# Performance work log

Measured on AMD Instinct MI355X. Metric: run time of the kernel, lower is better.

The kernel has to match this reference:

```python
import jax, jax.numpy as jnp
import numpy as np

NUM_CLASSES = 1000
DENSE_DIM = 64 * 64  # 4096, hardcoded in the module
BATCH = 8192
W0, W1 = 0.5, 0.5  # self.weights


def setup_inputs() -> dict:
    key = jax.random.key(0)
    k1, k2, k3, k4 = jax.random.split(key, 4)
    logits = jax.random.normal(k1, (BATCH, NUM_CLASSES), dtype=jnp.float32)
    dense_out = jax.random.normal(k2, (BATCH, DENSE_DIM), dtype=jnp.float32)
    target = jax.random.randint(k3, (BATCH,), 0, NUM_CLASSES, dtype=jnp.int32)
    # dense_labels buffer: random 0/1 per (class, dense) cell, as in __init__
    dense_labels = jax.random.bernoulli(k4, 0.5, (NUM_CLASSES, DENSE_DIM)).astype(jnp.float32)
    return {"logits": logits, "dense_out": dense_out, "target": target,
            "dense_labels": dense_labels}


def _bce_with_logits_mean(x, y):
    # numerically stable BCEWithLogitsLoss (mean reduction)
    return jnp.mean(jnp.maximum(x, 0.0) - x * y + jnp.log1p(jnp.exp(-jnp.abs(x))))


def reference(logits, dense_out, target, dense_labels):
    # --- accumulation (detached in the original; side-effect state) ---
    probs = jax.lax.stop_gradient(jax.nn.sigmoid(dense_out))  # [B, D]
    dense_output_sum = jax.ops.segment_sum(probs, target, num_segments=NUM_CLASSES)  # [C, D]
    total_accumulated = jax.ops.segment_sum(
        jnp.ones((BATCH,), dtype=jnp.float32), target, num_segments=NUM_CLASSES)  # [C]

    # --- losses ---
    dense_target = dense_labels[target]  # per-sample gather of label rows [B, D]
    logp = jax.nn.log_softmax(logits, axis=-1)
    loss1 = -jnp.mean(jnp.take_along_axis(logp, target[:, None], axis=1))  # CrossEntropyLoss
    loss2 = _bce_with_logits_mean(dense_out, dense_target)
    loss = loss1 * W0 + loss2 * W1
    return loss, dense_output_sum, total_accumulated
```

## Files before the change

kernel.cpp:

```cpp
#include <hip/hip_runtime.h>
#include <math.h>

#define NC   1000
#define DD   4096
#define BB   8192

#define MAIN_BLOCKS (NC * 2)
#define CE_BLOCKS   (BB / 4)
#define TOT_BLOCKS  (MAIN_BLOCKS + CE_BLOCKS)
#define MAXN 144
#define NSLOT 32
#define LN2  0.69314718055994531f


#define ACCX(xv, aAcc, sAcc)                                                  \
    {                                                                         \
        float e   = __expf(-fabsf(xv));                                       \
        float p1  = 1.f + e;                                                  \
        float inv = __builtin_amdgcn_rcpf(p1);                                \
        aAcc += (xv >= 0.f) ? inv : e * inv;                                  \
        sAcc += xv;                                                           \
        bceA += fmaxf(xv, 0.f);                                               \
        bceB += __log2f(p1);                                                  \
    }

__global__ __launch_bounds__(256, 4) void fused_k(const float* __restrict__ logits,
                                                  const float* __restrict__ dense_out,
                                                  const int*   __restrict__ target,
                                                  const float* __restrict__ dense_labels,
                                                  float* __restrict__ out,
                                                  double* __restrict__ loss1,
                                                  double* __restrict__ loss2) {
    int bx = blockIdx.x;
    int t  = threadIdx.x;
    int wave = t >> 6;
    int lane = t & 63;

    __shared__ int   sidx[MAXN];
    __shared__ int   s_n;
    __shared__ float red[4];

    bool is_main = ((bx & 1) == 0) && (bx < 2 * MAIN_BLOCKS);

    if (is_main) {
        int mb    = bx >> 1;
        int c     = mb >> 1;
        int chunk = mb & 1;
        int dbase = chunk * 2048 + (t << 2);

        if (t == 0) s_n = 0;
        __syncthreads();

        const float4* dpA = (const float4*)(dense_out + dbase);

        const int4* tp = (const int4*)target;
        #pragma unroll
        for (int k = 0; k < 8; ++k) {
            int4 v = tp[k * 256 + t];
            int s0 = (k * 256 + t) * 4;
            if (v.x == c) { int p = atomicAdd(&s_n, 1); sidx[p] = s0;     }
            if (v.y == c) { int p = atomicAdd(&s_n, 1); sidx[p] = s0 + 1; }
            if (v.z == c) { int p = atomicAdd(&s_n, 1); sidx[p] = s0 + 2; }
            if (v.w == c) { int p = atomicAdd(&s_n, 1); sidx[p] = s0 + 3; }
        }
        __syncthreads();
        int n  = s_n;
        int n2 = (n + 1) & ~1;
        if (t == 0 && n2 != n) sidx[n] = sidx[0];
        __syncthreads();

        float a0 = 0.f, a1 = 0.f, a2 = 0.f, a3 = 0.f;
        float a4 = 0.f, a5 = 0.f, a6 = 0.f, a7 = 0.f;
        float s0 = 0.f, s1 = 0.f, s2 = 0.f, s3 = 0.f;
        float s4 = 0.f, s5 = 0.f, s6 = 0.f, s7 = 0.f;
        float bceA = 0.f, bceB = 0.f;

        for (int base = 0; base < n2; base += 2) {
            int oA = sidx[base]     << 10;
            int oB = sidx[base + 1] << 10;
            float4 xa0 = dpA[oA];
            float4 xa1 = dpA[oA + 256];
            float4 xb0 = dpA[oB];
            float4 xb1 = dpA[oB + 256];

            ACCX(xa0.x, a0, s0) ACCX(xa0.y, a1, s1)
            ACCX(xa0.z, a2, s2) ACCX(xa0.w, a3, s3)
            ACCX(xa1.x, a4, s4) ACCX(xa1.y, a5, s5)
            ACCX(xa1.z, a6, s6) ACCX(xa1.w, a7, s7)
            if (base + 1 < n) {
                ACCX(xb0.x, a0, s0) ACCX(xb0.y, a1, s1)
                ACCX(xb0.z, a2, s2) ACCX(xb0.w, a3, s3)
                ACCX(xb1.x, a4, s4) ACCX(xb1.y, a5, s5)
                ACCX(xb1.z, a6, s6) ACCX(xb1.w, a7, s7)
            }
        }

        const float4* yp = (const float4*)(dense_labels + (size_t)c * DD + dbase);
        float4 y0 = yp[0];
        float4 y1 = yp[256];
        float bce = bceA + LN2 * bceB
                  - (y0.x * s0 + y0.y * s1 + y0.z * s2 + y0.w * s3
                   + y1.x * s4 + y1.y * s5 + y1.z * s6 + y1.w * s7);

        float* p = out + 1 + (size_t)c * DD + dbase;
        p[0] = a0; p[1] = a1; p[2] = a2; p[3] = a3;
        p[1024] = a4; p[1025] = a5; p[1026] = a6; p[1027] = a7;

        if (chunk == 0 && t == 0) out[1 + (size_t)NC * DD + c] = (float)n;

        #pragma unroll
        for (int o2 = 32; o2 > 0; o2 >>= 1) bce += __shfl_xor(bce, o2);
        if (lane == 0) red[wave] = bce;
        __syncthreads();
        if (t == 0)
            atomicAdd(&loss2[mb & (NSLOT - 1)],
                      (double)(red[0] + red[1] + red[2] + red[3]));
    } else {
        int ce_i = (bx < 2 * MAIN_BLOCKS) ? (bx >> 1) : (bx - MAIN_BLOCKS);
        int i = ce_i * 4 + wave;
        const float* row = logits + (size_t)i * NC;
        int j0 = lane * 4;

        float4 r0 = *(const float4*)(row + j0);
        float4 r1 = *(const float4*)(row + j0 + 256);
        float4 r2 = *(const float4*)(row + j0 + 512);
        float4 r3;
        if (j0 + 768 < NC) r3 = *(const float4*)(row + j0 + 768);
        else r3 = make_float4(-INFINITY, -INFINITY, -INFINITY, -INFINITY);
        float tl = row[target[i]];

        float mx = fmaxf(fmaxf(fmaxf(r0.x, r0.y), fmaxf(r0.z, r0.w)),
                         fmaxf(fmaxf(r1.x, r1.y), fmaxf(r1.z, r1.w)));
        mx = fmaxf(mx, fmaxf(fmaxf(r2.x, r2.y), fmaxf(r2.z, r2.w)));
        mx = fmaxf(mx, fmaxf(fmaxf(r3.x, r3.y), fmaxf(r3.z, r3.w)));
        #pragma unroll
        for (int o = 32; o > 0; o >>= 1) mx = fmaxf(mx, __shfl_xor(mx, o));

        float s = __expf(r0.x - mx) + __expf(r0.y - mx) + __expf(r0.z - mx) + __expf(r0.w - mx)
                + __expf(r1.x - mx) + __expf(r1.y - mx) + __expf(r1.z - mx) + __expf(r1.w - mx)
                + __expf(r2.x - mx) + __expf(r2.y - mx) + __expf(r2.z - mx) + __expf(r2.w - mx)
                + __expf(r3.x - mx) + __expf(r3.y - mx) + __expf(r3.z - mx) + __expf(r3.w - mx);
        #pragma unroll
        for (int o = 32; o > 0; o >>= 1) s += __shfl_xor(s, o);

        if (lane == 0) red[wave] = -(tl - mx - __logf(s));
        __syncthreads();
        if (t == 0)
            atomicAdd(&loss1[ce_i & (NSLOT - 1)],
                      (double)(red[0] + red[1] + red[2] + red[3]));
    }
}

__global__ void fin_k(const double* __restrict__ loss1,
                      const double* __restrict__ loss2,
                      float* __restrict__ out) {
    double l1 = 0.0, l2 = 0.0;
    #pragma unroll
    for (int i = 0; i < NSLOT; ++i) { l1 += loss1[i]; l2 += loss2[i]; }
    out[0] = (float)(0.5 * (l1 / (double)BB) +
                     0.5 * (l2 / ((double)BB * (double)DD)));
}

extern "C" void kernel_launch(void* const* d_in, const int* in_sizes, int n_in,
                              void* d_out, int out_size, void* d_ws, size_t ws_size,
                              hipStream_t stream) {
    const float* logits       = (const float*)d_in[0];
    const float* dense_out    = (const float*)d_in[1];
    const int*   target       = (const int*)d_in[2];
    const float* dense_labels = (const float*)d_in[3];
    float* out = (float*)d_out;

    char* ws = (char*)d_ws;
    double* loss1 = (double*)(ws + 0);
    double* loss2 = (double*)(ws + 256);

    hipMemsetAsync(d_ws, 0, 512, stream);

    fused_k<<<TOT_BLOCKS, 256, 0, stream>>>(logits, dense_out, target,
                                            dense_labels, out, loss1, loss2);
    fin_k<<<1, 1, 0, stream>>>(loss1, loss2, out);
}
```

Measured before the change: 255.9 us.

## Double-buffer gathered dense rows through LDS with async global_load_lds

Replaces direct per-thread float4 loads of the gathered dense_out rows with asynchronous global-to-LDS loads into a two-slot shared buffer. The next pair of rows is prefetched while the current pair is processed, with vmcnt waits to hold back reads until the data has landed. This hides global memory latency in the per-class gather loop. The cost is 32KB of extra LDS per block, which may limit occupancy (launch bounds ask for 4 blocks per CU). Each thread only reads back its own LDS slots, so no barrier is needed.

Measured after the change: 258.0 us. No clear change (+0.9%).

```diff
diff --git a/kernel.cpp b/kernel.cpp
--- a/kernel.cpp
+++ b/kernel.cpp
@@ -22,6 +22,27 @@
         sAcc += xv;                                                           \
         bceA += fmaxf(xv, 0.f);                                               \
         bceB += __log2f(p1);                                                  \
+    }
+
+#define STAGE2(bb, bs)                                                        \
+    {                                                                         \
+        int rA_ = sidx[(bb)];                                                 \
+        int rB_ = sidx[(bb) + 1];                                             \
+        const float* g0_ = gbase + ((size_t)rA_ << 12) + tof;                 \
+        const float* g2_ = gbase + ((size_t)rB_ << 12) + tof;                 \
+        float* l_ = xbuf + (bs) * 4096 + tof;                                 \
+        __builtin_amdgcn_global_load_lds(                                     \
+            (const __attribute__((address_space(1))) unsigned int*)(g0_),     \
+            (__attribute__((address_space(3))) unsigned int*)(l_), 16, 0, 0); \
+        __builtin_amdgcn_global_load_lds(                                     \
+            (const __attribute__((address_space(1))) unsigned int*)(g0_ + 1024),\
+            (__attribute__((address_space(3))) unsigned int*)(l_ + 1024), 16, 0, 0);\
+        __builtin_amdgcn_global_load_lds(                                     \
+            (const __attribute__((address_space(1))) unsigned int*)(g2_),     \
+            (__attribute__((address_space(3))) unsigned int*)(l_ + 2048), 16, 0, 0);\
+        __builtin_amdgcn_global_load_lds(                                     \
+            (const __attribute__((address_space(1))) unsigned int*)(g2_ + 1024),\
+            (__attribute__((address_space(3))) unsigned int*)(l_ + 3072), 16, 0, 0);\
     }
 
 __global__ __launch_bounds__(256, 4) void fused_k(const float* __restrict__ logits,
@@ -36,6 +57,7 @@
     int wave = t >> 6;
     int lane = t & 63;
 
+    __shared__ float xbuf[8192];
     __shared__ int   sidx[MAXN];
     __shared__ int   s_n;
     __shared__ float red[4];
@@ -51,7 +73,8 @@
         if (t == 0) s_n = 0;
         __syncthreads();
 
-        const float4* dpA = (const float4*)(dense_out + dbase);
+        const float* gbase = dense_out + chunk * 2048;
+        int tof = t << 2;
 
         const int4* tp = (const int4*)target;
         #pragma unroll
@@ -75,23 +98,34 @@
         float s4 = 0.f, s5 = 0.f, s6 = 0.f, s7 = 0.f;
         float bceA = 0.f, bceB = 0.f;
 
-        for (int base = 0; base < n2; base += 2) {
-            int oA = sidx[base]     << 10;
-            int oB = sidx[base + 1] << 10;
-            float4 xa0 = dpA[oA];
-            float4 xa1 = dpA[oA + 256];
-            float4 xb0 = dpA[oB];
-            float4 xb1 = dpA[oB + 256];
-
-            ACCX(xa0.x, a0, s0) ACCX(xa0.y, a1, s1)
-            ACCX(xa0.z, a2, s2) ACCX(xa0.w, a3, s3)
-            ACCX(xa1.x, a4, s4) ACCX(xa1.y, a5, s5)
-            ACCX(xa1.z, a6, s6) ACCX(xa1.w, a7, s7)
-            if (base + 1 < n) {
-                ACCX(xb0.x, a0, s0) ACCX(xb0.y, a1, s1)
-                ACCX(xb0.z, a2, s2) ACCX(xb0.w, a3, s3)
-                ACCX(xb1.x, a4, s4) ACCX(xb1.y, a5, s5)
-                ACCX(xb1.z, a6, s6) ACCX(xb1.w, a7, s7)
+        if (n2 > 0) {
+            STAGE2(0, 0);
+            int bsel = 0;
+            for (int base = 0; base < n2; base += 2) {
+                bool more = (base + 2) < n2;
+                if (more) {
+                    STAGE2(base + 2, bsel ^ 1);
+                    asm volatile("s_waitcnt vmcnt(4)" ::: "memory");
+                } else {
+                    asm volatile("s_waitcnt vmcnt(0)" ::: "memory");
+                }
+                const float4* b4 = (const float4*)(xbuf + bsel * 4096);
+                float4 x0 = b4[t];
+                float4 x1 = b4[256 + t];
+                float4 x2 = b4[512 + t];
+                float4 x3 = b4[768 + t];
+
+                ACCX(x0.x, a0, s0) ACCX(x0.y, a1, s1)
+                ACCX(x0.z, a2, s2) ACCX(x0.w, a3, s3)
+                ACCX(x1.x, a4, s4) ACCX(x1.y, a5, s5)
+                ACCX(x1.z, a6, s6) ACCX(x1.w, a7, s7)
+                if (base + 1 < n) {
+                    ACCX(x2.x, a0, s0) ACCX(x2.y, a1, s1)
+                    ACCX(x2.z, a2, s2) ACCX(x2.w, a3, s3)
+                    ACCX(x3.x, a4, s4) ACCX(x3.y, a5, s5)
+                    ACCX(x3.z, a6, s6) ACCX(x3.w, a7, s7)
+                }
+                bsel ^= 1;
             }
         }
 
```
